# Kernel tuning notes

Hardware: AMD Instinct MI355X
Metric: run time of the kernel (lower is better)

Reference implementation:

```python
import math
import jax
import jax.numpy as jnp
import numpy as np

NBINS = 9
POOL = 8
MAX_ANGLE = math.pi


def setup_inputs() -> dict:
    key = jax.random.key(0)
    x = jax.random.normal(key, (32, 3, 512, 512), dtype=jnp.float32)
    sob = jnp.array([[1.0, 0.0, -1.0], [2.0, 0.0, -2.0], [1.0, 0.0, -1.0]], dtype=jnp.float32)
    # weight: [2, 1, 3, 3] -> (sobel_x, sobel_y) over a single (channel-averaged) input channel
    weight = jnp.stack([sob, sob.T], axis=0)[:, None, :, :]
    return {"x": x, "weight": weight}


def reference(x, weight):
    # grayscale: mean over channels (module does this when C > 1)
    xg = x.mean(axis=1, keepdims=True)  # [n, 1, h, w]
    # 3x3 conv, stride 1, padding 1 -> gxy: [n, 2, h, w]
    gxy = jax.lax.conv_general_dilated(xg, weight, window_strides=(1, 1),
                                       padding=((1, 1), (1, 1)))
    gx, gy = gxy[:, 0], gxy[:, 1]
    norm = jnp.sqrt(gx * gx + gy * gy)          # [n, h, w] == gxy.norm(dim=1)
    phase = jnp.arctan2(gx, gy)                 # [n, h, w]
    phase_bin = phase / MAX_ANGLE * NBINS       # continuous bin coordinate
    lo = jnp.floor(phase_bin).astype(jnp.int32) % NBINS  # scatter_ (set) index
    hi = jnp.ceil(phase_bin).astype(jnp.int32) % NBINS   # scatter_add_ index
    bins = jnp.arange(NBINS, dtype=jnp.int32)[None, :, None, None]
    # scatter_(set norm at lo) then scatter_add_(1-norm at hi): since lo has a
    # single write per (n,h,w) onto zeros, the result equals the one-hot sum
    # (and when lo == hi, norm + (1 - norm) = 1, matching set-then-add).
    out = (jnp.where(lo[:, None] == bins, norm[:, None], 0.0)
           + jnp.where(hi[:, None] == bins, 1.0 - norm[:, None], 0.0))  # [n, nbins, h, w]
    n, b, h, w = out.shape
    # AvgPool2d(pool, stride=pool): h, w divisible by POOL
    return out.reshape(n, b, h // POOL, POOL, w // POOL, POOL).mean(axis=(3, 5))
```

## Files before the change

kernel.cpp:

```cpp
#include <hip/hip_runtime.h>
#include <math.h>

#define IMG_H 512
#define IMG_W 512
#define PLANE (IMG_H * IMG_W)
#define NB 9
#define LSTR 264

typedef __attribute__((ext_vector_type(2))) float f32x2;

__device__ __forceinline__ f32x2 fma2(f32x2 a, f32x2 b, f32x2 c) {
    return __builtin_elementwise_fma(a, b, c);
}
__device__ __forceinline__ f32x2 splat2(float v) { return (f32x2){v, v}; }

__device__ __forceinline__ f32x2 div3x2(f32x2 s) {
    const f32x2 y0 = splat2(0.33333334f);
    const f32x2 q  = s * y0;
    const f32x2 r  = fma2(splat2(-3.0f), q, s);
    return fma2(r, y0, q);
}
__device__ __forceinline__ float div3(float s) {
    const float y0 = 0.33333334f;
    const float q  = s * y0;
    const float r  = fmaf(-3.0f, q, s);
    return fmaf(r, y0, q);
}

__global__ __launch_bounds__(256, 4) void hog_kernel(const float* __restrict__ x,
                                                     float* __restrict__ out) {
    __shared__ float sgray[10 * LSTR];
    __shared__ float sbins[256 * NB];

    const int t    = threadIdx.x;
    const int n    = blockIdx.x >> 7;
    const int r7   = blockIdx.x & 127;
    const int cy   = r7 >> 1;
    const int half = r7 & 1;
    const int h0   = cy * 8;
    const int wstart = half * 256;
    const float* xn = x + (size_t)n * 3 * PLANE;

    if (t < 20) {
        const int r    = t >> 1;
        const int side = t & 1;
        const int h    = h0 - 1 + r;
        const int col  = wstart - 1 + side * 257;
        float g = 0.0f;
        if ((unsigned)h < IMG_H && (unsigned)col < IMG_W) {
            const float* p = xn + (size_t)h * IMG_W + col;
            g = div3((p[0] + p[PLANE]) + p[2 * PLANE]);
        }
        sgray[r * LSTR + 3 + side * 257] = g;
    }
#pragma unroll
    for (int k = 0; k < 3; k++) {
        const int i4 = t + k * 256;
        if (i4 < 640) {
            const int r  = i4 >> 6;
            const int c4 = i4 & 63;
            const int h  = h0 - 1 + r;
            float4 gv = make_float4(0.0f, 0.0f, 0.0f, 0.0f);
            if ((unsigned)h < IMG_H) {
                const float* p = xn + (size_t)h * IMG_W + wstart + 4 * c4;
                const float4 a = *(const float4*)(p);
                const float4 b = *(const float4*)(p + PLANE);
                const float4 c = *(const float4*)(p + 2 * PLANE);
                const f32x2* a2 = (const f32x2*)&a;
                const f32x2* b2 = (const f32x2*)&b;
                const f32x2* c2 = (const f32x2*)&c;
                const f32x2 g0 = div3x2((a2[0] + b2[0]) + c2[0]);
                const f32x2 g1 = div3x2((a2[1] + b2[1]) + c2[1]);
                gv = make_float4(g0.x, g0.y, g1.x, g1.y);
            }
            *(float4*)&sgray[r * LSTR + 4 + 4 * c4] = gv;
        }
    }
    __syncthreads();

#define PIXEL2(WA, WB, WC, LA, LB, W0A, W1A, W0B, W1B)                           \
    {                                                                            \
        const f32x2 tl = WA[0], tcv = WA[1], tr = WA[2];                         \
        const f32x2 ml = WB[0],               mr = WB[2];                        \
        const f32x2 bl = WC[0], bcv = WC[1], br = WC[2];                         \
        const f32x2 gx = ((((tl - tr) + 2.0f * ml) - 2.0f * mr) + bl) - br;      \
        const f32x2 gy = ((((tl + 2.0f * tcv) + tr) - bl) - 2.0f * bcv) - br;    \
        const f32x2 s2v = fma2(gx, gx, gy * gy);                                 \
        float nA, nB;                                                            \
        { float sa = s2v.x, sb = s2v.y;                                          \
          asm("v_sqrt_f32 %0, %1" : "=v"(nA) : "v"(sa));                         \
          asm("v_sqrt_f32 %0, %1" : "=v"(nB) : "v"(sb)); }                       \
        const float faA = fabsf(gx.x), fbA = fabsf(gy.x);                        \
        const float faB = fabsf(gx.y), fbB = fabsf(gy.y);                        \
        const float mnA = fminf(faA, fbA), mxA = fmaxf(faA, fbA);                \
        const float mnB = fminf(faB, fbB), mxB = fmaxf(faB, fbB);                \
        float rA, rB;                                                            \
        asm("v_rcp_f32 %0, %1" : "=v"(rA) : "v"(mxA));                           \
        asm("v_rcp_f32 %0, %1" : "=v"(rB) : "v"(mxB));                           \
        const f32x2 tt = (f32x2){mnA, mnB} * (f32x2){rA, rB};                    \
        const f32x2 ssv = tt * tt;                                               \
        f32x2 po = fma2(ssv, splat2(-0.03357890f), splat2(0.15084052f));         \
        po = fma2(ssv, po, splat2(-0.33355581f));                                \
        po = fma2(ssv, po, splat2(0.55446223f));                                 \
        po = fma2(ssv, po, splat2(-0.95289958f));                                \
        po = fma2(ssv, po, splat2(2.86472384f));         \
        const f32x2 w   = tt * po;                            \
        const f32x2 w45 = splat2(4.5f) - w;                                      \
        const float vA = (faA > fbA) ? w45.x : w.x;                              \
        const float vB = (faB > fbB) ? w45.y : w.y;                              \
        const f32x2 vv = (f32x2){vA, vB};                                        \
        const f32x2 v9 = splat2(9.0f) - vv;                                      \
        const int sxA = (int)(__float_as_uint(gx.x) ^ __float_as_uint(gy.x));    \
        const int sxB = (int)(__float_as_uint(gx.y) ^ __float_as_uint(gy.y));    \
        const float upA = (sxA < 0) ? v9.x : vA;                                 \
        const float upB = (sxB < 0) ? v9.y : vB;                                 \
        const f32x2 up2 = (f32x2){upA, upB};                                     \
        const f32x2 rn2 = (f32x2){__builtin_rintf(upA), __builtin_rintf(upB)};   \
        const f32x2 d2  = up2 - rn2;                                             \
        if (fabsf(d2.x) > 1.2e-4f) {                   \
            LA = (int)upA; W0A = nA; W1A = 1.0f - nA;                            \
        } else {                                                                 \
                       \
            const float ph  = (float)atan2((double)gx.x, (double)gy.x);          \
            const float pbf = ph / (float)M_PI * 9.0f;                           \
            int lo = (int)floorf(pbf) % NB; if (lo < 0) lo += NB;                \
            int hi = (int)ceilf(pbf)  % NB; if (hi < 0) hi += NB;                \
            LA = lo;                                                             \
            if (lo == hi) { W0A = nA + (1.0f - nA); W1A = 0.0f; }                \
            else          { W0A = nA; W1A = 1.0f - nA; }                         \
        }                                                                        \
        if (fabsf(d2.y) > 1.2e-4f) {                                             \
            LB = (int)upB; W0B = nB; W1B = 1.0f - nB;                            \
        } else {                                                                 \
            const float ph  = (float)atan2((double)gx.y, (double)gy.y);          \
            const float pbf = ph / (float)M_PI * 9.0f;                           \
            int lo = (int)floorf(pbf) % NB; if (lo < 0) lo += NB;                \
            int hi = (int)ceilf(pbf)  % NB; if (hi < 0) hi += NB;                \
            LB = lo;                                                             \
            if (lo == hi) { W0B = nB + (1.0f - nB); W1B = 0.0f; }                \
            else          { W0B = nB; W1B = 1.0f - nB; }                         \
        }                                                                        \
    }

    f32x2 bins2[NB];
#pragma unroll
    for (int b = 0; b < NB; b++) bins2[b] = splat2(0.0f);

    f32x2 wa[3], wb[3], wc[3];
    {
        const float* p0 = &sgray[0 * LSTR + t];
        const float* p1 = &sgray[1 * LSTR + t];
        const float* p4 = &sgray[4 * LSTR + t];
        const float* p5 = &sgray[5 * LSTR + t];
#pragma unroll
        for (int i = 0; i < 3; i++) {
            wa[i] = (f32x2){p0[3 + i], p4[3 + i]};
            wb[i] = (f32x2){p1[3 + i], p5[3 + i]};
        }
    }

#pragma unroll
    for (int k = 0; k < 4; k++) {
        const float* pA = &sgray[(k + 2) * LSTR + t];
        const float* pB = &sgray[(k + 6) * LSTR + t];
#pragma unroll
        for (int i = 0; i < 3; i++) wc[i] = (f32x2){pA[3 + i], pB[3 + i]};

        int LA, LB; float W0A, W1A, W0B, W1B;
        PIXEL2(wa, wb, wc, LA, LB, W0A, W1A, W0B, W1B)

        const f32x2 w0 = (f32x2){W0A, W0B};
        const f32x2 w1 = (f32x2){W1A, W1B};
        f32x2 sel[NB];
#pragma unroll
        for (int b = 0; b < NB; b++)
            sel[b] = (f32x2){(LA == b) ? 1.0f : 0.0f, (LB == b) ? 1.0f : 0.0f};
#pragma unroll
        for (int b = 0; b < NB; b++)
            bins2[b] = fma2(sel[b], w0, bins2[b]);
#pragma unroll
        for (int b = 0; b < NB; b++)
            bins2[b] = fma2(sel[(b + 8) % 9], w1, bins2[b]);

#pragma unroll
        for (int q = 0; q < 3; q++) { wa[q] = wb[q]; wb[q] = wc[q]; }
    }
#undef PIXEL2

    float* mybins = &sbins[t * NB];
#pragma unroll
    for (int b = 0; b < NB; b++) mybins[b] = bins2[b].x + bins2[b].y;
    __syncthreads();

    for (int idx = t; idx < NB * 32; idx += 256) {
        const int b  = idx >> 5;
        const int cc = idx & 31;
        const int base = 8 * cc * NB + b;
        float s = sbins[base];
#pragma unroll
        for (int j = 1; j < 8; j++) s += sbins[base + j * NB];
        out[((size_t)n * NB + b) * 4096 + (size_t)cy * 64 + half * 32 + cc]
            = s * (1.0f / 64.0f);
    }
}

extern "C" void kernel_launch(void* const* d_in, const int* in_sizes, int n_in,
                              void* d_out, int out_size, void* d_ws, size_t ws_size,
                              hipStream_t stream) {
    const float* x = (const float*)d_in[0];
    float* out = (float*)d_out;
    hog_kernel<<<4096, 256, 0, stream>>>(x, out);
}
```

Baseline: 32.92 us.

## Retile blocks to 16x128 regions and swizzle block order across images

Each block now covers a 16-row by 128-column tile instead of 8 rows by 256 columns, with the two halves of the thread block handling the upper and lower 8-row bands. That cuts the halo rows loaded per output pixel from 2/8 to 2/16, at the cost of more halo columns per tile. Block indices are also remapped with an interleave across groups of 8 (vb = (bid&7)*512 + bid>>3), which changes which tiles run at the same time and so alters cache and channel locality. The final pooling reduction is reindexed to match the new tile shape.

```diff
diff --git a/kernel.cpp b/kernel.cpp
--- a/kernel.cpp
+++ b/kernel.cpp
@@ -5,7 +5,7 @@
 #define IMG_W 512
 #define PLANE (IMG_H * IMG_W)
 #define NB 9
-#define LSTR 264
+#define LSTR 136
 
 typedef __attribute__((ext_vector_type(2))) float f32x2;
 
@@ -29,46 +29,51 @@
 
 __global__ __launch_bounds__(256, 4) void hog_kernel(const float* __restrict__ x,
                                                      float* __restrict__ out) {
-    __shared__ float sgray[10 * LSTR];
+    __shared__ float sgray[18 * LSTR];
     __shared__ float sbins[256 * NB];
 
-    const int t    = threadIdx.x;
-    const int n    = blockIdx.x >> 7;
-    const int r7   = blockIdx.x & 127;
-    const int cy   = r7 >> 1;
-    const int half = r7 & 1;
-    const int h0   = cy * 8;
-    const int wstart = half * 256;
+    const int t  = threadIdx.x;
+    const int vb   = (blockIdx.x & 7) * 512 + (blockIdx.x >> 3);
+    const int n    = vb >> 7;
+    const int rem  = vb & 127;
+    const int band = rem >> 2;
+    const int grp  = rem & 3;
+    const int th0  = band * 16;
+    const int wstart = grp * 128;
     const float* xn = x + (size_t)n * 3 * PLANE;
 
-    if (t < 20) {
+    const int c  = t & 127;
+    const int rh = t >> 7;
+    const int rbase = rh * 8;
+
+    if (t < 36) {
         const int r    = t >> 1;
         const int side = t & 1;
-        const int h    = h0 - 1 + r;
-        const int col  = wstart - 1 + side * 257;
+        const int h    = th0 - 1 + r;
+        const int col  = wstart - 1 + side * 129;
         float g = 0.0f;
         if ((unsigned)h < IMG_H && (unsigned)col < IMG_W) {
             const float* p = xn + (size_t)h * IMG_W + col;
             g = div3((p[0] + p[PLANE]) + p[2 * PLANE]);
         }
-        sgray[r * LSTR + 3 + side * 257] = g;
+        sgray[r * LSTR + 3 + side * 129] = g;
     }
 #pragma unroll
     for (int k = 0; k < 3; k++) {
         const int i4 = t + k * 256;
-        if (i4 < 640) {
-            const int r  = i4 >> 6;
-            const int c4 = i4 & 63;
-            const int h  = h0 - 1 + r;
+        if (i4 < 576) {
+            const int r  = i4 >> 5;
+            const int c4 = i4 & 31;
+            const int h  = th0 - 1 + r;
             float4 gv = make_float4(0.0f, 0.0f, 0.0f, 0.0f);
             if ((unsigned)h < IMG_H) {
                 const float* p = xn + (size_t)h * IMG_W + wstart + 4 * c4;
                 const float4 a = *(const float4*)(p);
                 const float4 b = *(const float4*)(p + PLANE);
-                const float4 c = *(const float4*)(p + 2 * PLANE);
+                const float4 cc = *(const float4*)(p + 2 * PLANE);
                 const f32x2* a2 = (const f32x2*)&a;
                 const f32x2* b2 = (const f32x2*)&b;
-                const f32x2* c2 = (const f32x2*)&c;
+                const f32x2* c2 = (const f32x2*)&cc;
                 const f32x2 g0 = div3x2((a2[0] + b2[0]) + c2[0]);
                 const f32x2 g1 = div3x2((a2[1] + b2[1]) + c2[1]);
                 gv = make_float4(g0.x, g0.y, g1.x, g1.y);
@@ -104,7 +109,7 @@
         po = fma2(ssv, po, splat2(0.55446223f));                                 \
         po = fma2(ssv, po, splat2(-0.95289958f));                                \
         po = fma2(ssv, po, splat2(2.86472384f));         \
-        const f32x2 w   = tt * po;                            \
+        const f32x2 w   = tt * po;                                               \
         const f32x2 w45 = splat2(4.5f) - w;                                      \
         const float vA = (faA > fbA) ? w45.x : w.x;                              \
         const float vB = (faB > fbB) ? w45.y : w.y;                              \
@@ -120,7 +125,6 @@
         if (fabsf(d2.x) > 1.2e-4f) {                   \
             LA = (int)upA; W0A = nA; W1A = 1.0f - nA;                            \
         } else {                                                                 \
-                       \
             const float ph  = (float)atan2((double)gx.x, (double)gy.x);          \
             const float pbf = ph / (float)M_PI * 9.0f;                           \
             int lo = (int)floorf(pbf) % NB; if (lo < 0) lo += NB;                \
@@ -148,10 +152,10 @@
 
     f32x2 wa[3], wb[3], wc[3];
     {
-        const float* p0 = &sgray[0 * LSTR + t];
-        const float* p1 = &sgray[1 * LSTR + t];
-        const float* p4 = &sgray[4 * LSTR + t];
-        const float* p5 = &sgray[5 * LSTR + t];
+        const float* p0 = &sgray[(rbase + 0) * LSTR + c];
+        const float* p1 = &sgray[(rbase + 1) * LSTR + c];
+        const float* p4 = &sgray[(rbase + 4) * LSTR + c];
+        const float* p5 = &sgray[(rbase + 5) * LSTR + c];
 #pragma unroll
         for (int i = 0; i < 3; i++) {
             wa[i] = (f32x2){p0[3 + i], p4[3 + i]};
@@ -161,8 +165,8 @@
 
 #pragma unroll
     for (int k = 0; k < 4; k++) {
-        const float* pA = &sgray[(k + 2) * LSTR + t];
-        const float* pB = &sgray[(k + 6) * LSTR + t];
+        const float* pA = &sgray[(rbase + k + 2) * LSTR + c];
+        const float* pB = &sgray[(rbase + k + 6) * LSTR + c];
 #pragma unroll
         for (int i = 0; i < 3; i++) wc[i] = (f32x2){pA[3 + i], pB[3 + i]};
 
@@ -193,14 +197,16 @@
     __syncthreads();
 
     for (int idx = t; idx < NB * 32; idx += 256) {
-        const int b  = idx >> 5;
-        const int cc = idx & 31;
-        const int base = 8 * cc * NB + b;
+        const int b   = idx >> 5;
+        const int cel = idx & 31;
+        const int crh = cel >> 4;
+        const int cc  = cel & 15;
+        const int base = (crh * 128 + 8 * cc) * NB + b;
         float s = sbins[base];
 #pragma unroll
         for (int j = 1; j < 8; j++) s += sbins[base + j * NB];
-        out[((size_t)n * NB + b) * 4096 + (size_t)cy * 64 + half * 32 + cc]
-            = s * (1.0f / 64.0f);
+        out[((size_t)n * NB + b) * 4096 + (size_t)(band * 2 + crh) * 64
+            + grp * 16 + cc] = s * (1.0f / 64.0f);
     }
 }
 
```

Measured after the change: 29.38 us, median of 2. -10.8%, faster.
